# Kernel tuning notes

Hardware: AMD Instinct MI355X
Metric: run time of the kernel (lower is better)

The kernel has to match this reference:

```python
import jax, jax.numpy as jnp
import numpy as np

EMBED = 1024
HEADS = 16
HEAD_DIM = EMBED // HEADS
HIDDEN = 4096
EPS = 1e-5


def setup_inputs() -> dict:
    key = jax.random.key(0)
    ks = jax.random.split(key, 12)
    s_e = 1.0 / np.sqrt(EMBED)
    s_h = 1.0 / np.sqrt(HIDDEN)
    inp = {
        'x': jax.random.normal(ks[0], (2, 2048, EMBED), jnp.float32),
        'Wq': jax.random.uniform(ks[1], (EMBED, EMBED), jnp.float32, -s_e, s_e),
        'bq': jnp.zeros((EMBED,), jnp.float32),
        'Wk': jax.random.uniform(ks[2], (EMBED, EMBED), jnp.float32, -s_e, s_e),
        'bk': jnp.zeros((EMBED,), jnp.float32),
        'Wv': jax.random.uniform(ks[3], (EMBED, EMBED), jnp.float32, -s_e, s_e),
        'bv': jnp.zeros((EMBED,), jnp.float32),
        'Wo': jax.random.uniform(ks[4], (EMBED, EMBED), jnp.float32, -s_e, s_e),
        'bo': jnp.zeros((EMBED,), jnp.float32),
        'g1': jnp.ones((EMBED,), jnp.float32),
        'b1': jnp.zeros((EMBED,), jnp.float32),
        'W1': jax.random.uniform(ks[5], (EMBED, HIDDEN), jnp.float32, -s_e, s_e),
        'bm1': jnp.zeros((HIDDEN,), jnp.float32),
        'W2': jax.random.uniform(ks[6], (HIDDEN, EMBED), jnp.float32, -s_h, s_h),
        'bm2': jnp.zeros((EMBED,), jnp.float32),
        'g2': jnp.ones((EMBED,), jnp.float32),
        'b2': jnp.zeros((EMBED,), jnp.float32),
    }
    return inp


def _layernorm(x, g, b):
    mu = jnp.mean(x, axis=-1, keepdims=True)
    var = jnp.mean(jnp.square(x - mu), axis=-1, keepdims=True)
    return (x - mu) * jax.lax.rsqrt(var + EPS) * g + b


def _attention(x, Wq, bq, Wk, bk, Wv, bv, Wo, bo):
    b, n, d = x.shape
    def split(h):  # [b,n,d] -> [b,H,n,hd]
        return h.reshape(b, n, HEADS, HEAD_DIM).transpose(0, 2, 1, 3)
    q = split(x @ Wq + bq)
    k = split(x @ Wk + bk)
    v = split(x @ Wv + bv)
    # NOTE: original multiplies by sqrt(head_dim) (bug preserved for faithfulness)
    scores = jnp.einsum('bhqd,bhkd->bhqk', q, k) * jnp.sqrt(jnp.float32(HEAD_DIM))
    causal = jnp.tril(jnp.ones((n, n), bool))
    scores = jnp.where(causal, scores, -jnp.inf)
    attn = jax.nn.softmax(scores, axis=-1)
    out = jnp.einsum('bhqk,bhkd->bhqd', attn, v)
    out = out.transpose(0, 2, 1, 3).reshape(b, n, d)
    return out @ Wo + bo


def reference(x, Wq, bq, Wk, bk, Wv, bv, Wo, bo, g1, b1, W1, bm1, W2, bm2, g2, b2):
    res1 = x
    x = _layernorm(_attention(x, Wq, bq, Wk, bk, Wv, bv, Wo, bo), g1, b1) + res1
    res2 = x
    h = jax.nn.gelu(x @ W1 + bm1, approximate=False) @ W2 + bm2
    return _layernorm(h, g2, b2) + res2
```

## Files before the change

### kernel.cpp

```cpp
#include <hip/hip_runtime.h>
#include <stdint.h>

typedef unsigned short u16;
typedef short short8 __attribute__((ext_vector_type(8)));
typedef float f32x4 __attribute__((ext_vector_type(4)));
typedef u16 u16x4 __attribute__((ext_vector_type(4)));
typedef u16 u16x8 __attribute__((ext_vector_type(8)));

#define MODE_F32  0
#define MODE_GELU 2
#define MODE_VT   4

#define QSCALE 11.5415603271f

__device__ __forceinline__ float b2f(u16 v) {
    union { uint32_t u; float f; } x; x.u = ((uint32_t)v) << 16; return x.f;
}
__device__ __forceinline__ u16 f2b(float f) {
    union { float f; uint32_t u; } x; x.f = f;
    uint32_t u = x.u;
    return (u16)((u + 0x7FFFu + ((u >> 16) & 1u)) >> 16);
}
__device__ __forceinline__ u16 f2b_trunc(float f) {
    union { float f; uint32_t u; } x; x.f = f;
    return (u16)(x.u >> 16);
}

#define ASYNC16(gp, lp)                                                        \
    __builtin_amdgcn_global_load_lds(                                          \
        (const __attribute__((address_space(1))) uint32_t*)(const void*)(gp),  \
        (__attribute__((address_space(3))) uint32_t*)(void*)(lp), 16, 0, 0)

#define MFMA16(a, b, c) __builtin_amdgcn_mfma_f32_16x16x32_bf16((a), (b), (c), 0, 0, 0)

__global__ __launch_bounds__(256) void split_f32(
    const float* __restrict__ in, u16* __restrict__ hi, u16* __restrict__ lo)
{
    const int i = (blockIdx.x * 256 + threadIdx.x) * 4;
    f32x4 v = *(const f32x4*)&in[i];
    u16x4 h, l;
    for (int k = 0; k < 4; k++) {
        h[k] = f2b(v[k]);
        l[k] = f2b(v[k] - b2f(h[k]));
    }
    *(u16x4*)&hi[i] = h;
    *(u16x4*)&lo[i] = l;
}

__global__ __launch_bounds__(256) void transpose_f32_bf16(
    const float* __restrict__ inA, u16* __restrict__ outA,
    const float* __restrict__ inB, u16* __restrict__ outB, int rows, int cols)
{
    const float* in = blockIdx.z ? inB : inA;
    u16* out = blockIdx.z ? outB : outA;
    __shared__ float t[32][33];
    const int r0 = blockIdx.y * 32, c0 = blockIdx.x * 32;
    const int tr = threadIdx.x >> 3, tc = (threadIdx.x & 7) * 4;
    f32x4 v = *(const f32x4*)&in[(size_t)(r0 + tr) * cols + c0 + tc];
    for (int i = 0; i < 4; i++) t[tr][tc + i] = v[i];
    __syncthreads();
    u16x4 ov;
    for (int i = 0; i < 4; i++) ov[i] = f2b(t[tc + i][tr]);
    *(u16x4*)&out[(size_t)(c0 + tr) * rows + r0 + tc] = ov;
}

__global__ __launch_bounds__(256) void transpose_split_f32(
    const float* __restrict__ inA, u16* __restrict__ hiA, u16* __restrict__ loA,
    const float* __restrict__ inB, u16* __restrict__ hiB, u16* __restrict__ loB,
    int rows, int cols)
{
    const float* in = blockIdx.z ? inB : inA;
    u16* hi = blockIdx.z ? hiB : hiA;
    u16* lo = blockIdx.z ? loB : loA;
    __shared__ float t[32][33];
    const int r0 = blockIdx.y * 32, c0 = blockIdx.x * 32;
    const int tr = threadIdx.x >> 3, tc = (threadIdx.x & 7) * 4;
    f32x4 v = *(const f32x4*)&in[(size_t)(r0 + tr) * cols + c0 + tc];
    for (int i = 0; i < 4; i++) t[tr][tc + i] = v[i];
    __syncthreads();
    u16x4 hv, lv;
    for (int i = 0; i < 4; i++) {
        const float f = t[tc + i][tr];
        hv[i] = f2b(f);
        lv[i] = f2b(f - b2f(hv[i]));
    }
    const size_t o = (size_t)(c0 + tr) * rows + r0 + tc;
    *(u16x4*)&hi[o] = hv;
    *(u16x4*)&lo[o] = lv;
}

__global__ __launch_bounds__(512) void gemm_qk_x3(
    const u16* __restrict__ Ahi, const u16* __restrict__ Alo,
    const u16* __restrict__ Bhi, const u16* __restrict__ Blo,
    const float* __restrict__ bq, const float* __restrict__ bk,
    u16* __restrict__ Qhi, u16* __restrict__ Qlo,
    u16* __restrict__ Khi, u16* __restrict__ Klo)
{
    const int K = 1024;
    __shared__ __align__(16) u16 SM[32768];
    u16* lAh = SM;          u16* lAl = SM + 8192;
    u16* lBh = SM + 16384;  u16* lBl = SM + 24576;

    const int tid = threadIdx.x;
    const int w = tid >> 6, lane = tid & 63;
    const int lane15 = lane & 15, q = lane >> 4;
    const int tM = blockIdx.y * 128, tN = blockIdx.x * 128;
    const int m0 = (w >> 1) * 32, n0 = (w & 1) * 64;

    f32x4 acc[2][4];
    for (int i = 0; i < 2; i++)
        for (int j = 0; j < 4; j++)
            acc[i][j] = (f32x4){0.f, 0.f, 0.f, 0.f};

    const int srow = lane >> 2, sch = lane & 3;
    const u16* Ah = Ahi + (size_t)tM * K;
    const u16* Al = Alo + (size_t)tM * K;
    const u16* Bh = Bhi + (size_t)tN * K;
    const u16* Bl = Blo + (size_t)tN * K;

    #define STAGE_QK(buf_off, k0)                                              \
        for (int ii = 0; ii < 4; ii++) {                                       \
            const int id = w * 4 + ii, op = id >> 3, ch = id & 7;              \
            const u16* src = op == 0 ? Ah : op == 1 ? Al : op == 2 ? Bh : Bl;  \
            u16* dst = op == 0 ? lAh : op == 1 ? lAl : op == 2 ? lBh : lBl;    \
            ASYNC16(src + (size_t)(ch * 16 + srow) * K + (k0) + sch * 8,       \
                    dst + (buf_off) + ch * 512);                               \
        }

    STAGE_QK(0, 0)

    const int NT = K / 32;
    for (int kt = 0; kt < NT; kt++) {
        __syncthreads();
        const int cb = (kt & 1) * 4096, nb = 4096 - cb;
        if (kt + 1 < NT) {
            const int k0 = (kt + 1) * 32;
            STAGE_QK(nb, k0)
        }
        short8 afh[2], afl[2], bfh[4], bfl[4];
        for (int i = 0; i < 2; i++) {
            const int o = cb + (m0 + i * 16 + lane15) * 32 + q * 8;
            afh[i] = *(const short8*)&lAh[o];
            afl[i] = *(const short8*)&lAl[o];
        }
        for (int j = 0; j < 4; j++) {
            const int o = cb + (n0 + j * 16 + lane15) * 32 + q * 8;
            bfh[j] = *(const short8*)&lBh[o];
            bfl[j] = *(const short8*)&lBl[o];
        }
        for (int i = 0; i < 2; i++)
            for (int j = 0; j < 4; j++) {
                acc[i][j] = MFMA16(afh[i], bfh[j], acc[i][j]);
                acc[i][j] = MFMA16(afh[i], bfl[j], acc[i][j]);
                acc[i][j] = MFMA16(afl[i], bfh[j], acc[i][j]);
            }
    }

    const bool isQ = (tN < 1024);
    u16* dhi = isQ ? Qhi : Khi;
    u16* dlo = isQ ? Qlo : Klo;
    const int cN = isQ ? tN : (tN - 1024);
    const float scl = isQ ? QSCALE : 1.0f;
    u16* sC = SM;
    for (int pass = 0; pass < 2; pass++) {
        __syncthreads();
        for (int i = 0; i < 2; i++) {
            const int rl0 = m0 + i * 16 + q * 4;
            for (int j = 0; j < 4; j++) {
                const int cl = n0 + j * 16 + lane15;
                const float bv = isQ ? bq[cN + cl] : bk[cN + cl];
                for (int r = 0; r < 4; r++) {
                    const float v = (acc[i][j][r] + bv) * scl;
                    const u16 hv = f2b(v);
                    sC[(rl0 + r) * 136 + cl] = pass == 0 ? hv : f2b(v - b2f(hv));
                }
            }
        }
        __syncthreads();
        u16* dst = pass == 0 ? dhi : dlo;
        for (int t8 = 0; t8 < 4; t8++) {
            const int rl = t8 * 32 + (tid >> 4), cl = (tid & 15) * 8;
            *(u16x8*)&dst[(size_t)(tM + rl) * 1024 + cN + cl] = *(const u16x8*)&sC[rl * 136 + cl];
        }
    }
}

__global__ __launch_bounds__(512) void gemm_bt(
    const u16* __restrict__ A, const u16* __restrict__ Bt, const float* __restrict__ bias,
    int M, int N, int K, int mode,
    float* __restrict__ outF, u16* __restrict__ outB, size_t pstride)
{
    __shared__ __align__(16) u16 SM[17408];
    u16* lA = SM;
    u16* lB = SM + 8192;

    const int tid = threadIdx.x;
    const int w = tid >> 6, lane = tid & 63;
    const int lane15 = lane & 15, q = lane >> 4;
    const int tM = blockIdx.y * 128, tN = blockIdx.x * 128;
    const int m0 = (w >> 1) * 32, n0 = (w & 1) * 64;

    const int kchunk = K / gridDim.z;
    const int koff = blockIdx.z * kchunk;
    outF += (size_t)blockIdx.z * pstride;

    f32x4 acc[2][4];
    for (int i = 0; i < 2; i++)
        for (int j = 0; j < 4; j++)
            acc[i][j] = (f32x4){0.f, 0.f, 0.f, 0.f};

    const int srow = lane >> 2, sch = lane & 3;
    const u16* Abase = A + (size_t)tM * K + koff;
    const u16* Bbase = Bt + (size_t)tN * K + koff;
    #define STAGE_BT(buf_off, k0)                                              \
        for (int ii = 0; ii < 2; ii++) {                                       \
            const int id = w * 2 + ii;                                         \
            const u16* src = id < 8 ? Abase : Bbase;                           \
            u16* dst = id < 8 ? lA : lB;                                       \
            const int ch = id & 7;                                             \
            ASYNC16(src + (size_t)(ch * 16 + srow) * K + (k0) + sch * 8,       \
                    dst + (buf_off) + ch * 512);                               \
        }

    STAGE_BT(0, 0)

    const int NT = kchunk / 32;
    for (int kt = 0; kt < NT; kt++) {
        __syncthreads();
        const int cb = (kt & 1) * 4096, nb = 4096 - cb;
        if (kt + 1 < NT) {
            const int k0 = (kt + 1) * 32;
            STAGE_BT(nb, k0)
        }
        short8 af[2], bf[4];
        for (int i = 0; i < 2; i++) af[i] = *(const short8*)&lA[cb + (m0 + i * 16 + lane15) * 32 + q * 8];
        for (int j = 0; j < 4; j++) bf[j] = *(const short8*)&lB[cb + (n0 + j * 16 + lane15) * 32 + q * 8];
        for (int i = 0; i < 2; i++)
            for (int j = 0; j < 4; j++)
                acc[i][j] = MFMA16(af[i], bf[j], acc[i][j]);
    }

    if (mode == MODE_F32) {
        for (int i = 0; i < 2; i++) {
            const int rb = tM + m0 + i * 16 + q * 4;
            for (int j = 0; j < 4; j++) {
                const int col = tN + n0 + j * 16 + lane15;
                const float bv = (bias && blockIdx.z == 0) ? bias[col] : 0.f;
                for (int r = 0; r < 4; r++)
                    outF[(size_t)(rb + r) * N + col] = acc[i][j][r] + bv;
            }
        }
        return;
    }

    u16* sC = SM;
    __syncthreads();
    if (mode == MODE_GELU) {
        for (int i = 0; i < 2; i++) {
            const int rl0 = m0 + i * 16 + q * 4;
            for (int j = 0; j < 4; j++) {
                const int cl = n0 + j * 16 + lane15;
                const float bv = bias[tN + cl];
                for (int r = 0; r < 4; r++) {
                    float v = acc[i][j][r] + bv;
                    v = 0.5f * v * (1.f + erff(v * 0.70710678118f));
                    sC[(rl0 + r) * 136 + cl] = f2b(v);
                }
            }
        }
        __syncthreads();
        for (int t8 = 0; t8 < 4; t8++) {
            const int rl = t8 * 32 + (tid >> 4), cl = (tid & 15) * 8;
            *(u16x8*)&outB[(size_t)(tM + rl) * N + tN + cl] = *(const u16x8*)&sC[rl * 136 + cl];
        }
    } else {
        for (int i = 0; i < 2; i++) {
            const int rl0 = m0 + i * 16 + q * 4;
            for (int j = 0; j < 4; j++) {
                const int cl = n0 + j * 16 + lane15;
                const float bv = bias[tN + cl];
                for (int r = 0; r < 4; r++)
                    sC[cl * 136 + rl0 + r] = f2b(acc[i][j][r] + bv);
            }
        }
        __syncthreads();
        const int bb = tM >> 11, nbase = tM & 2047;
        for (int t8 = 0; t8 < 4; t8++) {
            const int cl = t8 * 32 + (tid >> 4), rl = (tid & 15) * 8;
            const int colg = tN + cl;
            u16* dst = &outB[((size_t)(bb * 16 + (colg >> 6)) * 64 + (colg & 63)) * 2048 + nbase + rl];
            *(u16x8*)dst = *(const u16x8*)&sC[cl * 136 + rl];
        }
    }
}

__global__ __launch_bounds__(256) void gemm_bt4(
    const u16* __restrict__ A, const u16* __restrict__ Bt, const float* __restrict__ bias,
    int M, int N, int K, int mode,
    float* __restrict__ outF, u16* __restrict__ outB, size_t pstride)
{
    __shared__ __align__(16) u16 SM[17408];
    u16* lA = SM;
    u16* lB = SM + 8192;

    const int tid = threadIdx.x;
    const int w = tid >> 6, lane = tid & 63;
    const int lane15 = lane & 15, q = lane >> 4;
    const int tM = blockIdx.y * 128, tN = blockIdx.x * 128;
    const int m0 = (w >> 1) * 64, n0 = (w & 1) * 64;

    const int kchunk = K / gridDim.z;
    const int koff = blockIdx.z * kchunk;
    outF += (size_t)blockIdx.z * pstride;

    f32x4 acc[4][4];
    for (int i = 0; i < 4; i++)
        for (int j = 0; j < 4; j++)
            acc[i][j] = (f32x4){0.f, 0.f, 0.f, 0.f};

    const int srow = lane >> 2, sch = lane & 3;
    const u16* Abase = A + (size_t)tM * K + koff;
    const u16* Bbase = Bt + (size_t)tN * K + koff;
#define STAGE_BT4(buf_off, k0)                                                 \
    for (int ii = 0; ii < 4; ii++) {                                           \
        const int id = w * 4 + ii;                                             \
        const u16* src = id < 8 ? Abase : Bbase;                               \
        u16* dst = id < 8 ? lA : lB;                                           \
        const int ch = id & 7;                                                 \
        ASYNC16(src + (size_t)(ch * 16 + srow) * K + (k0) + sch * 8,           \
                dst + (buf_off) + ch * 512);                                   \
    }

    STAGE_BT4(0, 0)

    const int NT = kchunk / 32;
    for (int kt = 0; kt < NT; kt++) {
        __syncthreads();
        const int cb = (kt & 1) * 4096, nb = 4096 - cb;
        if (kt + 1 < NT) {
            const int k0 = (kt + 1) * 32;
            STAGE_BT4(nb, k0)
        }
        short8 af[4], bf[4];
        for (int i = 0; i < 4; i++)
            af[i] = *(const short8*)&lA[cb + (m0 + i * 16 + lane15) * 32 + q * 8];
        for (int j = 0; j < 4; j++)
            bf[j] = *(const short8*)&lB[cb + (n0 + j * 16 + lane15) * 32 + q * 8];
        for (int i = 0; i < 4; i++)
            for (int j = 0; j < 4; j++)
                acc[i][j] = MFMA16(af[i], bf[j], acc[i][j]);
    }

    if (mode == MODE_F32) {
        for (int i = 0; i < 4; i++) {
            const int rb = tM + m0 + i * 16 + q * 4;
            for (int j = 0; j < 4; j++) {
                const int col = tN + n0 + j * 16 + lane15;
                const float bv = (bias && blockIdx.z == 0) ? bias[col] : 0.f;
                for (int r = 0; r < 4; r++)
                    outF[(size_t)(rb + r) * N + col] = acc[i][j][r] + bv;
            }
        }
        return;
    }

    u16* sC = SM;
    __syncthreads();
    for (int i = 0; i < 4; i++) {
        const int rl0 = m0 + i * 16 + q * 4;
        for (int j = 0; j < 4; j++) {
            const int cl = n0 + j * 16 + lane15;
            const float bv = bias[tN + cl];
            for (int r = 0; r < 4; r++) {
                float v = acc[i][j][r] + bv;
                v = 0.5f * v * (1.f + erff(v * 0.70710678118f));
                sC[(rl0 + r) * 136 + cl] = f2b(v);
            }
        }
    }
    __syncthreads();
    for (int t8 = 0; t8 < 8; t8++) {
        const int rl = t8 * 16 + (tid >> 4), cl = (tid & 15) * 8;
        *(u16x8*)&outB[(size_t)(tM + rl) * N + tN + cl] = *(const u16x8*)&sC[rl * 136 + cl];
    }
}

__global__ __launch_bounds__(256) void attn_fwd(
    const u16* __restrict__ Qhig, const u16* __restrict__ Qlog,
    const u16* __restrict__ Khig, const u16* __restrict__ Klog,
    const u16* __restrict__ Vtg, u16* __restrict__ Og)
{
    __shared__ __align__(16) u16 lKh[2][4096];
    __shared__ __align__(16) u16 lKl[2][4096];
    __shared__ __align__(16) u16 lV [2][4096];
    __shared__ __align__(16) u16 lPb[4][1152];

    const int tid = threadIdx.x, w = tid >> 6, lane = tid & 63;
    const int lane15 = lane & 15, q = lane >> 4;
    const int bh = blockIdx.x & 31;
    const int pr = blockIdx.x >> 5;
    const int b = bh >> 4, h = bh & 15;

    const size_t xoff = (size_t)b * 2048 * 1024 + h * 64;
    const u16* Qh_ = Qhig + xoff;
    const u16* Ql_ = Qlog + xoff;
    const u16* Kh_ = Khig + xoff;
    const u16* Kl_ = Klog + xoff;
    const u16* Vbh = Vtg + (size_t)bh * 64 * 2048;
    u16* Obh = Og + xoff;

    u16* lP = lPb[w];
    const float NEG = -3.0e38f;
    const float THR = 11.5415603271f;

    const int rsub = lane >> 3;
    const int csw  = ((lane & 7) ^ rsub) * 8;
    const int swz  = (lane15 & 7) << 3;

    short8 ones;
    for (int i = 0; i < 8; i++) ones[i] = (short)0x3F80;

#define STAGE_KV(buf, k0)                                                      \
    for (int ii = 0; ii < 6; ii++) {                                           \
        const int id = w * 6 + ii, sel = id >> 3, c = id & 7;                  \
        if (sel == 0)                                                          \
            ASYNC16(Kh_ + (size_t)((k0) + c * 8 + rsub) * 1024 + csw,          \
                    &lKh[buf][c * 512]);                                       \
        else if (sel == 1)                                                     \
            ASYNC16(Kl_ + (size_t)((k0) + c * 8 + rsub) * 1024 + csw,          \
                    &lKl[buf][c * 512]);                                       \
        else                                                                   \
            ASYNC16(Vbh + (size_t)(c * 8 + rsub) * 2048 + (k0) + csw,          \
                    &lV[buf][c * 512]);                                        \
    }

    for (int ph = 0; ph < 2; ph++) {
        const int qb = ph ? (31 - pr) : pr;
        const int qrow0 = qb * 64;
        const int wrow0 = qrow0 + w * 16;
        const int ntiles = qb + 1;

        const size_t qro = (size_t)(wrow0 + lane15) * 1024;
        short8 aqh0 = *(const short8*)&Qh_[qro + q * 8];
        short8 aqh1 = *(const short8*)&Qh_[qro + 32 + q * 8];
        short8 aql0 = *(const short8*)&Ql_[qro + q * 8];
        short8 aql1 = *(const short8*)&Ql_[qro + 32 + q * 8];

        if (ph) __syncthreads();
        STAGE_KV(0, 0)

        f32x4 o[4];
        for (int j = 0; j < 4; j++) o[j] = (f32x4){0.f, 0.f, 0.f, 0.f};
        float mrow[4], lrow[4];
        for (int r = 0; r < 4; r++) { mrow[r] = NEG; lrow[r] = 0.f; }

        for (int t = 0; t < ntiles; t++) {
            __syncthreads();
            const int cur = t & 1, nxt = cur ^ 1;
            if (t + 1 < ntiles) {
                STAGE_KV(nxt, (t + 1) * 64)
            }
            const int kk0 = t * 64;

            f32x4 s[4];
            for (int sub = 0; sub < 4; sub++) {
                const int kb = (sub * 16 + lane15) * 64;
                short8 bkh0 = *(const short8*)&lKh[cur][kb + ((q * 8) ^ swz)];
                short8 bkh1 = *(const short8*)&lKh[cur][kb + ((32 + q * 8) ^ swz)];
                short8 bkl0 = *(const short8*)&lKl[cur][kb + ((q * 8) ^ swz)];
                short8 bkl1 = *(const short8*)&lKl[cur][kb + ((32 + q * 8) ^ swz)];
                f32x4 z = (f32x4){0.f, 0.f, 0.f, 0.f};
                z = MFMA16(aqh0, bkh0, z);
                z = MFMA16(aqh1, bkh1, z);
                z = MFMA16(aqh0, bkl0, z);
                z = MFMA16(aqh1, bkl1, z);
                z = MFMA16(aql0, bkh0, z);
                z = MFMA16(aql1, bkh1, z);
                s[sub] = z;
            }
            if (t == ntiles - 1) {
                const int rbase = wrow0 + q * 4;
                for (int sub = 0; sub < 4; sub++)
                    for (int r = 0; r < 4; r++) {
                        const int key = kk0 + sub * 16 + lane15;
                        if (key > rbase + r) s[sub][r] = NEG;
                    }
            }
            float mx[4];
            for (int r = 0; r < 4; r++)
                mx[r] = fmaxf(fmaxf(s[0][r], s[1][r]), fmaxf(s[2][r], s[3][r]));
            for (int d = 1; d < 16; d <<= 1)
                for (int r = 0; r < 4; r++) mx[r] = fmaxf(mx[r], __shfl_xor(mx[r], d));
            bool need = false;
            for (int r = 0; r < 4; r++) need |= (mx[r] > mrow[r] + THR);
            if (__any(need)) {
                for (int r = 0; r < 4; r++) {
                    const float mnew = fmaxf(mrow[r], mx[r]);
                    const float alpha = __builtin_exp2f(mrow[r] - mnew);
                    mrow[r] = mnew;
                    lrow[r] *= alpha;
                    for (int j = 0; j < 4; j++) o[j][r] *= alpha;
                }
            }
            for (int sub = 0; sub < 4; sub++)
                for (int r = 0; r < 4; r++) {
                    const float p = __builtin_exp2f(s[sub][r] - mrow[r]);
                    lP[(q * 4 + r) * 72 + sub * 16 + lane15] = f2b_trunc(p);
                }
            short8 ap0 = *(const short8*)&lP[lane15 * 72 + q * 8];
            short8 ap1 = *(const short8*)&lP[lane15 * 72 + 32 + q * 8];
            f32x4 zs = (f32x4){0.f, 0.f, 0.f, 0.f};
            zs = MFMA16(ap0, ones, zs);
            zs = MFMA16(ap1, ones, zs);
            for (int r = 0; r < 4; r++) lrow[r] += zs[r];
            for (int j = 0; j < 4; j++) {
                const int vb = (j * 16 + lane15) * 64;
                short8 bv0 = *(const short8*)&lV[cur][vb + ((q * 8) ^ swz)];
                short8 bv1 = *(const short8*)&lV[cur][vb + ((32 + q * 8) ^ swz)];
                o[j] = MFMA16(ap0, bv0, o[j]);
                o[j] = MFMA16(ap1, bv1, o[j]);
            }
        }
        float inv[4];
        for (int r = 0; r < 4; r++) inv[r] = 1.0f / lrow[r];
        for (int j = 0; j < 4; j++)
            for (int r = 0; r < 4; r++)
                Obh[(size_t)(wrow0 + q * 4 + r) * 1024 + j * 16 + lane15] =
                    f2b(o[j][r] * inv[r]);
    }
#undef STAGE_KV
}

__global__ __launch_bounds__(256) void ln_res(
    const float* __restrict__ Xa, const float* __restrict__ Xb,
    const float* __restrict__ resF, const u16* __restrict__ resB,
    const float* __restrict__ g, const float* __restrict__ bb,
    u16* __restrict__ outB, float* __restrict__ outF)
{
    const int w = threadIdx.x >> 6, lane = threadIdx.x & 63;
    const int row = blockIdx.x * 4 + w;
    const size_t rowo = (size_t)row * 1024;
    f32x4 v[4];
    float s = 0.f, ss = 0.f;
    for (int i = 0; i < 4; i++) {
        const int c0 = (i * 64 + lane) * 4;
        v[i] = *(const f32x4*)&Xa[rowo + c0];
        if (Xb) {
            f32x4 v2 = *(const f32x4*)&Xb[rowo + c0];
            for (int k = 0; k < 4; k++) v[i][k] += v2[k];
        }
        for (int k = 0; k < 4; k++) { s += v[i][k]; ss += v[i][k] * v[i][k]; }
    }
    for (int d = 1; d < 64; d <<= 1) { s += __shfl_xor(s, d); ss += __shfl_xor(ss, d); }
    const float mu = s * (1.f / 1024.f);
    const float var = ss * (1.f / 1024.f) - mu * mu;
    const float rstd = rsqrtf(var + 1e-5f);
    for (int i = 0; i < 4; i++) {
        const int c0 = (i * 64 + lane) * 4;
        f32x4 gv = *(const f32x4*)&g[c0];
        f32x4 bv = *(const f32x4*)&bb[c0];
        f32x4 rv;
        if (resF) rv = *(const f32x4*)&resF[rowo + c0];
        else {
            u16x4 rb = *(const u16x4*)&resB[rowo + c0];
            for (int k = 0; k < 4; k++) rv[k] = b2f(rb[k]);
        }
        f32x4 ov;
        for (int k = 0; k < 4; k++)
            ov[k] = (v[i][k] - mu) * rstd * gv[k] + bv[k] + rv[k];
        if (outF) *(f32x4*)&outF[rowo + c0] = ov;
        if (outB) {
            u16x4 ob;
            for (int k = 0; k < 4; k++) ob[k] = f2b(ov[k]);
            *(u16x4*)&outB[rowo + c0] = ob;
        }
    }
}

extern "C" void kernel_launch(void* const* d_in, const int* in_sizes, int n_in,
                              void* d_out, int out_size, void* d_ws, size_t ws_size,
                              hipStream_t stream)
{
    const float* x   = (const float*)d_in[0];
    const float* Wq  = (const float*)d_in[1];  const float* bq  = (const float*)d_in[2];
    const float* Wk  = (const float*)d_in[3];  const float* bk  = (const float*)d_in[4];
    const float* Wv  = (const float*)d_in[5];  const float* bv  = (const float*)d_in[6];
    const float* Wo  = (const float*)d_in[7];  const float* bo  = (const float*)d_in[8];
    const float* g1  = (const float*)d_in[9];  const float* b1  = (const float*)d_in[10];
    const float* W1  = (const float*)d_in[11]; const float* bm1 = (const float*)d_in[12];
    const float* W2  = (const float*)d_in[13]; const float* bm2 = (const float*)d_in[14];
    const float* g2  = (const float*)d_in[15]; const float* b2  = (const float*)d_in[16];

    const size_t MB = (size_t)1 << 20;
    char* ws = (char*)d_ws;
    u16* xhi    = (u16*)(ws + 0 * MB);
    u16* xlo    = (u16*)(ws + 8 * MB);
    u16* WqkThi = (u16*)(ws + 16 * MB);
    u16* WqkTlo = (u16*)(ws + 20 * MB);
    u16* WvT    = (u16*)(ws + 24 * MB);
    u16* WoT    = (u16*)(ws + 26 * MB);
    u16* W1T    = (u16*)(ws + 32 * MB);
    u16* W2T    = (u16*)(ws + 40 * MB);
    u16* Qhi    = (u16*)(ws + 48 * MB);
    u16* Qlo    = (u16*)(ws + 56 * MB);
    u16* Khi    = (u16*)(ws + 64 * MB);
    u16* Klo    = (u16*)(ws + 72 * MB);
    u16* Vtb    = (u16*)(ws + 80 * MB);
    u16* aout   = (u16*)(ws + 16 * MB);
    float* O1   = (float*)(ws + 48 * MB);
    float* O2   = (float*)(ws + 64 * MB);
    u16* x1b    = (u16*)(ws + 80 * MB);
    u16* Hb     = (u16*)(ws + 0 * MB);
    float* H2a  = (float*)(ws + 48 * MB);
    float* H2b  = (float*)(ws + 64 * MB);

    split_f32<<<4096, 256, 0, stream>>>(x, xhi, xlo);
    transpose_split_f32<<<dim3(32, 32, 2), 256, 0, stream>>>(
        Wq, WqkThi, WqkTlo,
        Wk, WqkThi + 1024 * 1024, WqkTlo + 1024 * 1024, 1024, 1024);
    transpose_f32_bf16<<<dim3(32, 32, 2), 256, 0, stream>>>(Wv, WvT, Wo, WoT, 1024, 1024);
    transpose_f32_bf16<<<dim3(128, 32), 256, 0, stream>>>(W1, W1T, nullptr, nullptr, 1024, 4096);
    transpose_f32_bf16<<<dim3(32, 128), 256, 0, stream>>>(W2, W2T, nullptr, nullptr, 4096, 1024);

    gemm_qk_x3<<<dim3(16, 32), 512, 0, stream>>>(xhi, xlo, WqkThi, WqkTlo, bq, bk,
                                                 Qhi, Qlo, Khi, Klo);
    gemm_bt<<<dim3(8, 32), 512, 0, stream>>>(xhi, WvT, bv, 4096, 1024, 1024,
                                             MODE_VT, nullptr, Vtb, 0);

    attn_fwd<<<dim3(512), 256, 0, stream>>>(Qhi, Qlo, Khi, Klo, Vtb, aout);

    gemm_bt4<<<dim3(8, 32, 2), 256, 0, stream>>>(aout, WoT, bo, 4096, 1024, 1024,
                                                 MODE_F32, O1, nullptr, (size_t)16 * MB / 4);
    ln_res<<<1024, 256, 0, stream>>>(O1, O2, x, nullptr, g1, b1, x1b, nullptr);

    gemm_bt4<<<dim3(32, 32), 256, 0, stream>>>(x1b, W1T, bm1, 4096, 4096, 1024,
                                               MODE_GELU, nullptr, Hb, 0);
    gemm_bt4<<<dim3(8, 32, 2), 256, 0, stream>>>(Hb, W2T, bm2, 4096, 1024, 4096,
                                                 MODE_F32, H2a, nullptr, (size_t)16 * MB / 4);
    ln_res<<<1024, 256, 0, stream>>>(H2a, H2b, nullptr, x1b, g2, b2, nullptr, (float*)d_out);
}
```

Baseline: 432.5 us.

## Add dedicated 256x256-tile FFN1 GEMM with async double-buffered swizzled LDS

Replaces the generic 128x128 gemm_bt4 launch for the first FFN matmul (4096x4096x1024 with GELU) with a specialized kernel using 256x256 tiles, 512 threads, async global-to-LDS copies into XOR-swizzled double buffers, and a quadrant-ordered MFMA schedule with s_setprio. Larger tiles raise arithmetic intensity and cut global traffic, and the swizzle avoids LDS bank conflicts. The cost is 128KB of LDS per block and a grid of only 256 blocks, which lowers occupancy and may leave CUs underfilled. The epilogue is staged through LDS in 64-row passes.

```diff
diff --git a/kernel.cpp b/kernel.cpp
--- a/kernel.cpp
+++ b/kernel.cpp
@@ -383,6 +383,139 @@
         const int rl = t8 * 16 + (tid >> 4), cl = (tid & 15) * 8;
         *(u16x8*)&outB[(size_t)(tM + rl) * N + tN + cl] = *(const u16x8*)&sC[rl * 136 + cl];
     }
+}
+
+__global__ __launch_bounds__(512, 2) void gemm_ffn1(
+    const u16* __restrict__ A, const u16* __restrict__ Bt,
+    const float* __restrict__ bias, u16* __restrict__ outB)
+{
+    const int K = 1024, N = 4096;
+    __shared__ __align__(16) u16 lA[2][16384];
+    __shared__ __align__(16) u16 lB[2][16384];
+
+    const int tid = threadIdx.x, w = tid >> 6, lane = tid & 63;
+    const int lane15 = lane & 15, q = lane >> 4;
+    const int wm = w >> 2, wn = w & 3;
+    const int tM = blockIdx.y * 256, tN = blockIdx.x * 256;
+    const int rsub = lane >> 3;
+    const int csw = ((lane & 7) ^ rsub) * 8;
+
+    const u16* Ab = A + (size_t)tM * K;
+    const u16* Bb = Bt + (size_t)tN * K;
+
+#define STAGE_F1(buf, T)                                                       \
+    for (int l = 0; l < 8; l++) {                                              \
+        const int id = w * 8 + l, c = id & 31;                                 \
+        if (id < 32)                                                           \
+            ASYNC16(Ab + (size_t)(c * 8 + rsub) * K + (T) * 64 + csw,          \
+                    &lA[buf][c * 512]);                                        \
+        else                                                                   \
+            ASYNC16(Bb + (size_t)(c * 8 + rsub) * K + (T) * 64 + csw,          \
+                    &lB[buf][c * 512]);                                        \
+    }
+
+#define BARX() do { __builtin_amdgcn_s_barrier(); asm volatile("" ::: "memory"); } while (0)
+#define VMFENCE() asm volatile("s_waitcnt vmcnt(0)" ::: "memory")
+
+    f32x4 acc[8][4];
+    #pragma unroll
+    for (int i = 0; i < 8; i++)
+        #pragma unroll
+        for (int j = 0; j < 4; j++)
+            acc[i][j] = (f32x4){0.f, 0.f, 0.f, 0.f};
+
+    const int ar0 = wm * 128 + lane15;
+    const int br0 = wn * 64 + lane15;
+
+    short8 a[4][2], b[2][2];
+
+#define RD_B(buf, ch)                                                          \
+    _Pragma("unroll") for (int jj = 0; jj < 2; jj++)                           \
+    _Pragma("unroll") for (int kk = 0; kk < 2; kk++) {                         \
+        const int r = br0 + (ch) * 32 + jj * 16;                               \
+        b[jj][kk] = *(const short8*)                                           \
+            &lB[buf][r * 64 + ((kk * 32 + q * 8) ^ ((r & 7) << 3))];           \
+    }
+#define RD_A(buf, rh)                                                          \
+    _Pragma("unroll") for (int i = 0; i < 4; i++)                              \
+    _Pragma("unroll") for (int kk = 0; kk < 2; kk++) {                         \
+        const int r = ar0 + (rh) * 64 + i * 16;                                \
+        a[i][kk] = *(const short8*)                                            \
+            &lA[buf][r * 64 + ((kk * 32 + q * 8) ^ ((r & 7) << 3))];           \
+    }
+#define QUAD(RH, CH)                                                           \
+    __builtin_amdgcn_s_setprio(1);                                             \
+    _Pragma("unroll") for (int i = 0; i < 4; i++)                              \
+    _Pragma("unroll") for (int jj = 0; jj < 2; jj++) {                         \
+        acc[(RH)*4+i][(CH)*2+jj] =                                             \
+            MFMA16(a[i][0], b[jj][0], acc[(RH)*4+i][(CH)*2+jj]);               \
+        acc[(RH)*4+i][(CH)*2+jj] =                                             \
+            MFMA16(a[i][1], b[jj][1], acc[(RH)*4+i][(CH)*2+jj]);               \
+    }                                                                          \
+    __builtin_amdgcn_s_setprio(0);
+
+#define HALF(buf, STAGECODE)                                                   \
+    RD_B(buf, 0)                                                               \
+    RD_A(buf, 0)                                                               \
+    STAGECODE                                                                  \
+    BARX();                                                                    \
+    QUAD(0, 0)                                                                 \
+    BARX();                                                                    \
+    RD_B(buf, 1)                                                               \
+    QUAD(0, 1)                                                                 \
+    BARX();                                                                    \
+    RD_A(buf, 1)                                                               \
+    RD_B(buf, 0)                                                               \
+    QUAD(1, 0)                                                                 \
+    BARX();                                                                    \
+    RD_B(buf, 1)                                                               \
+    QUAD(1, 1)                                                                 \
+    VMFENCE();                                                                 \
+    BARX();
+
+    STAGE_F1(0, 0)
+    VMFENCE();
+    BARX();
+
+    for (int it = 0; it < 8; it++) {
+        const int T = 2 * it;
+        HALF(0, STAGE_F1(1, T + 1))
+        HALF(1, if (T + 2 < 16) { STAGE_F1(0, T + 2) })
+    }
+
+    u16* sC = &lA[0][0];
+    float bv[4];
+    #pragma unroll
+    for (int jj = 0; jj < 4; jj++)
+        bv[jj] = bias[tN + wn * 64 + jj * 16 + lane15];
+    for (int p = 0; p < 4; p++) {
+        if ((p >> 1) == wm) {
+            const int rh = p & 1;
+            #pragma unroll
+            for (int i = 0; i < 4; i++)
+                #pragma unroll
+                for (int jj = 0; jj < 4; jj++)
+                    #pragma unroll
+                    for (int r = 0; r < 4; r++) {
+                        float v = acc[rh * 4 + i][jj][r] + bv[jj];
+                        v = 0.5f * v * (1.f + erff(v * 0.70710678118f));
+                        sC[(i * 16 + q * 4 + r) * 264 + wn * 64 + jj * 16 + lane15] = f2b(v);
+                    }
+        }
+        __syncthreads();
+        #pragma unroll
+        for (int s = 0; s < 4; s++) {
+            const int row = s * 16 + (tid >> 5), colg = (tid & 31) * 8;
+            *(u16x8*)&outB[(size_t)(tM + p * 64 + row) * N + tN + colg] =
+                *(const u16x8*)&sC[row * 264 + colg];
+        }
+        __syncthreads();
+    }
+#undef STAGE_F1
+#undef RD_A
+#undef RD_B
+#undef QUAD
+#undef HALF
 }
 
 __global__ __launch_bounds__(256) void attn_fwd(
@@ -633,8 +766,7 @@
                                                  MODE_F32, O1, nullptr, (size_t)16 * MB / 4);
     ln_res<<<1024, 256, 0, stream>>>(O1, O2, x, nullptr, g1, b1, x1b, nullptr);
 
-    gemm_bt4<<<dim3(32, 32), 256, 0, stream>>>(x1b, W1T, bm1, 4096, 4096, 1024,
-                                               MODE_GELU, nullptr, Hb, 0);
+    gemm_ffn1<<<dim3(16, 16), 512, 0, stream>>>(x1b, W1T, bm1, Hb);
     gemm_bt4<<<dim3(8, 32, 2), 256, 0, stream>>>(Hb, W2T, bm2, 4096, 1024, 4096,
                                                  MODE_F32, H2a, nullptr, (size_t)16 * MB / 4);
     ln_res<<<1024, 256, 0, stream>>>(H2a, H2b, nullptr, x1b, g2, b2, nullptr, (float*)d_out);
```

New measurement: 517.2 us. 1.2x slower.
